# Kernel optimization log

Measured on AMD Instinct MI355X. Metric: run time of the kernel, lower is better.

## Reference

```python
import jax, jax.numpy as jnp
import numpy as np

B, S, H = 1, 2048, 2048
NH = 16
Q_LORA, KV_LORA = 1536, 512
D_NOPE, D_ROPE, D_V = 128, 64, 128
D_QK = D_NOPE + D_ROPE  # 192
EPS = 1e-6
ROPE_BASE = 10000.0


def setup_inputs() -> dict:
    key = jax.random.key(0)
    ks = jax.random.split(key, 8)
    def lin(k, fan_in, fan_out):
        # nn.Linear default init, stored as [in, out] for x @ W
        bound = 1.0 / np.sqrt(fan_in)
        return jax.random.uniform(k, (fan_in, fan_out), jnp.float32, -bound, bound)
    return {
        "hidden_states": jax.random.normal(ks[0], (B, S, H), jnp.float32),
        "Wqa": lin(ks[1], H, Q_LORA),
        "q_a_ln_w": jnp.ones((Q_LORA,), jnp.float32),
        "Wqb": lin(ks[2], Q_LORA, NH * D_QK),
        "Wkva": lin(ks[3], H, KV_LORA + D_ROPE),
        "kv_a_ln_w": jnp.ones((KV_LORA,), jnp.float32),
        "Wkvb": lin(ks[4], KV_LORA, NH * (D_NOPE + D_V)),
        "Wo": lin(ks[5], NH * D_V, H),
    }


def _rmsnorm(x, w):
    xf = x.astype(jnp.float32)
    var = jnp.mean(xf * xf, axis=-1, keepdims=True)
    return w * (xf * jax.lax.rsqrt(var + EPS)).astype(x.dtype)


def _rotate_half(x):
    x1, x2 = jnp.split(x, 2, axis=-1)
    return jnp.concatenate((-x2, x1), axis=-1)


def _rope_tables(seq_len, dtype=jnp.float32):
    inv_freq = 1.0 / (ROPE_BASE ** (jnp.arange(0, D_ROPE, 2, dtype=jnp.float32) / D_ROPE))
    t = jnp.arange(seq_len, dtype=jnp.float32)
    freqs = jnp.outer(t, inv_freq)                      # [S, D_ROPE/2]
    emb = jnp.concatenate((freqs, freqs), axis=-1)      # [S, D_ROPE]
    return jnp.cos(emb).astype(dtype), jnp.sin(emb).astype(dtype)


def reference(hidden_states, Wqa, q_a_ln_w, Wqb, Wkva, kv_a_ln_w, Wkvb, Wo):
    bsz, q_len, _ = hidden_states.shape
    scale = D_QK ** -0.5

    # Q path: LoRA down -> RMSNorm -> up
    q = _rmsnorm(hidden_states @ Wqa, q_a_ln_w) @ Wqb            # [B,S,NH*D_QK]
    q = q.reshape(bsz, q_len, NH, D_QK).transpose(0, 2, 1, 3)    # [B,NH,S,D_QK]
    q_nope, q_pe = q[..., :D_NOPE], q[..., D_NOPE:]

    # KV path: compressed latent + shared rope key
    ckv = hidden_states @ Wkva                                    # [B,S,KV_LORA+D_ROPE]
    compressed_kv, k_pe = ckv[..., :KV_LORA], ckv[..., KV_LORA:]
    k_pe = k_pe.reshape(bsz, q_len, 1, D_ROPE).transpose(0, 2, 1, 3)  # [B,1,S,D_ROPE]
    kv = _rmsnorm(compressed_kv, kv_a_ln_w) @ Wkvb                # [B,S,NH*(D_NOPE+D_V)]
    kv = kv.reshape(bsz, q_len, NH, D_NOPE + D_V).transpose(0, 2, 1, 3)
    k_nope, v = kv[..., :D_NOPE], kv[..., D_NOPE:]                # [B,NH,S,D_NOPE], [B,NH,S,D_V]

    # decoupled RoPE on the rope sub-dims
    cos, sin = _rope_tables(q_len, hidden_states.dtype)
    cos = cos[None, None]  # [1,1,S,D_ROPE] broadcast over batch & heads
    sin = sin[None, None]
    q_pe = q_pe * cos + _rotate_half(q_pe) * sin
    k_pe = k_pe * cos + _rotate_half(k_pe) * sin                  # [B,1,S,D_ROPE]

    query = jnp.concatenate([q_nope, q_pe], axis=-1)              # [B,NH,S,D_QK]
    key = jnp.concatenate([k_nope, jnp.broadcast_to(k_pe, (bsz, NH, q_len, D_ROPE))], axis=-1)

    attn = jnp.einsum('bhqd,bhkd->bhqk', query, key) * scale      # [B,NH,S,S]
    causal = jnp.triu(jnp.ones((q_len, q_len), bool), k=1)
    attn = jnp.where(causal, -jnp.inf, attn)
    attn = jax.nn.softmax(attn.astype(jnp.float32), axis=-1).astype(query.dtype)

    out = jnp.einsum('bhqk,bhkd->bhqd', attn, v)                  # [B,NH,S,D_V]
    out = out.transpose(0, 2, 1, 3).reshape(bsz, q_len, NH * D_V)
    return out @ Wo                                               # [B,S,H]
```

## Files before the change

kernel.cpp:

```cpp
#include <hip/hip_runtime.h>
#include <hip/hip_bf16.h>
#include <math.h>

#define S_LEN 2048
#define H_DIM 2048
#define NH 16
#define Q_LORA 1536
#define KV_LORA 512
#define D_NOPE 128
#define D_ROPE 64
#define D_V 128
#define D_QK 192

typedef unsigned short ushort_t;
typedef __attribute__((ext_vector_type(8))) short short8;
typedef __attribute__((ext_vector_type(4))) float f32x4;

__device__ __forceinline__ ushort_t f2bf(float f) {
    unsigned int u = __float_as_uint(f);
    u = (u + 0x7FFFu + ((u >> 16) & 1u)) >> 16;
    return (ushort_t)u;
}
__device__ __forceinline__ float bf2f(ushort_t u) {
    return __uint_as_float(((unsigned int)u) << 16);
}

__device__ __forceinline__ float exp2_fast(float x) {
    float r;
    asm volatile("v_exp_f32 %0, %1" : "=v"(r) : "v"(x));
    return r;
}

__device__ __forceinline__ void storeC(float* p, float v) { *p = v; }
__device__ __forceinline__ void storeC(ushort_t* p, float v) { *p = f2bf(v); }

__device__ __forceinline__ void gload_lds16(const ushort_t* g, ushort_t* l) {
    __builtin_amdgcn_global_load_lds(
        (const __attribute__((address_space(1))) unsigned int*)(const void*)g,
        (__attribute__((address_space(3))) unsigned int*)(void*)l, 16, 0, 0);
}

__device__ __forceinline__ float dpp_max16(float x) {
    x = fmaxf(x, __int_as_float(__builtin_amdgcn_update_dpp(0, __float_as_int(x), 0xB1, 0xF, 0xF, true)));
    x = fmaxf(x, __int_as_float(__builtin_amdgcn_update_dpp(0, __float_as_int(x), 0x4E, 0xF, 0xF, true)));
    x = fmaxf(x, __int_as_float(__builtin_amdgcn_update_dpp(0, __float_as_int(x), 0x124, 0xF, 0xF, true)));
    x = fmaxf(x, __int_as_float(__builtin_amdgcn_update_dpp(0, __float_as_int(x), 0x128, 0xF, 0xF, true)));
    return x;
}
__device__ __forceinline__ float dpp_sum16(float x) {
    x += __int_as_float(__builtin_amdgcn_update_dpp(0, __float_as_int(x), 0xB1, 0xF, 0xF, true));
    x += __int_as_float(__builtin_amdgcn_update_dpp(0, __float_as_int(x), 0x4E, 0xF, 0xF, true));
    x += __int_as_float(__builtin_amdgcn_update_dpp(0, __float_as_int(x), 0x124, 0xF, 0xF, true));
    x += __int_as_float(__builtin_amdgcn_update_dpp(0, __float_as_int(x), 0x128, 0xF, 0xF, true));
    return x;
}

__device__ __forceinline__ void convT_body(
    const float* __restrict__ W, ushort_t* __restrict__ Wt,
    int K, int N, int n0, int k0, float (*tile)[33])
{
    const int tr = threadIdx.x >> 5, tc = threadIdx.x & 31;
    #pragma unroll
    for (int i = 0; i < 4; ++i) {
        int r = tr + i * 8;
        float v = 0.f;
        if (n0 + tc < N) v = W[(size_t)(k0 + r) * N + n0 + tc];
        tile[r][tc] = v;
    }
    __syncthreads();
    #pragma unroll
    for (int i = 0; i < 4; ++i) {
        int r = tr + i * 8;
        Wt[(size_t)(n0 + r) * K + k0 + tc] = f2bf(tile[tc][r]);
    }
}

__global__ __launch_bounds__(256) void unified_conv(
    const float* __restrict__ hs, ushort_t* __restrict__ hs16,
    const float* __restrict__ Wqa, const float* __restrict__ Wkva,
    const float* __restrict__ Wqb, const float* __restrict__ Wkvb,
    const float* __restrict__ Wo,
    ushort_t* __restrict__ WcatT, ushort_t* __restrict__ WqbT,
    ushort_t* __restrict__ WkvbT, ushort_t* __restrict__ WoT)
{
    __shared__ float tile[32][33];
    int b = blockIdx.x;
    if (b < 4096) {
        int base = (b * 256 + threadIdx.x) * 4;
        float4 v = *(const float4*)(hs + base);
        hs16[base + 0] = f2bf(v.x);
        hs16[base + 1] = f2bf(v.y);
        hs16[base + 2] = f2bf(v.z);
        hs16[base + 3] = f2bf(v.w);
        return;
    }
    b -= 4096;
    const float* W; ushort_t* Wt; int K, N, nbx;
    if (b < 3072)        {            W = Wqa;  Wt = WcatT;                              K = 2048; N = 1536; nbx = 48;  }
    else if (b < 4352)   { b -= 3072; W = Wkva; Wt = WcatT + (size_t)Q_LORA * H_DIM;     K = 2048; N = 576;  nbx = 20;  }
    else if (b < 8960)   { b -= 4352; W = Wqb;  Wt = WqbT;                               K = 1536; N = 3072; nbx = 96;  }
    else if (b < 11008)  { b -= 8960; W = Wkvb; Wt = WkvbT;                              K = 512;  N = 4096; nbx = 128; }
    else                 { b -= 11008; W = Wo;  Wt = WoT;                                K = 2048; N = 2048; nbx = 64;  }
    convT_body(W, Wt, K, N, (b % nbx) * 32, (b / nbx) * 32, tile);
}

__global__ __launch_bounds__(256) void fused_norm_ropek(
    const ushort_t* __restrict__ cat16r, ushort_t* __restrict__ qa16,
    ushort_t* __restrict__ ckv16n, ushort_t* __restrict__ kpe16,
    const float* __restrict__ qlnw, const float* __restrict__ klnw)
{
    __shared__ float red[4];
    const int b = blockIdx.x;
    if (b < 4096) {
        const bool isQ = (b < 2048);
        const int row = isQ ? b : b - 2048;
        const int K = isQ ? Q_LORA : KV_LORA;
        const ushort_t* x = cat16r + (size_t)row * 2176 + (isQ ? 0 : Q_LORA);
        ushort_t* y = (isQ ? qa16 + (size_t)row * Q_LORA : ckv16n + (size_t)row * KV_LORA);
        const float* wv = isQ ? qlnw : klnw;
        float ss = 0.f;
        for (int i = threadIdx.x; i < K; i += 256) { float v = bf2f(x[i]); ss += v * v; }
        #pragma unroll
        for (int off = 32; off > 0; off >>= 1) ss += __shfl_down(ss, off);
        int lane = threadIdx.x & 63, wid = threadIdx.x >> 6;
        if (lane == 0) red[wid] = ss;
        __syncthreads();
        float tot = red[0] + red[1] + red[2] + red[3];
        float rs = rsqrtf(tot / (float)K + 1e-6f);
        for (int i = threadIdx.x; i < K; i += 256)
            y[i] = f2bf(bf2f(x[i]) * rs * wv[i]);
    } else {
        int idx = (b - 4096) * 256 + threadIdx.x;
        if (idx >= S_LEN * 32) return;
        int i = idx & 31;
        int s = idx >> 5;
        float inv = powf(10000.0f, -(2.0f * i) / 64.0f);
        float ang = (float)s * inv;
        float c = cosf(ang), sn = sinf(ang);
        const ushort_t* p = cat16r + (size_t)s * 2176 + Q_LORA + KV_LORA;
        ushort_t* q = kpe16 + (size_t)s * D_ROPE;
        float x1 = bf2f(p[i]), x2 = bf2f(p[i + 32]);
        q[i]      = f2bf(x1 * c - x2 * sn);
        q[i + 32] = f2bf(x2 * c + x1 * sn);
    }
}

__global__ __launch_bounds__(256) void conv_vT_kernel(
    const ushort_t* __restrict__ kv, ushort_t* __restrict__ v16t)
{
    __shared__ ushort_t tile[32][33];
    const int h = blockIdx.z;
    const int s0 = blockIdx.x * 32, d0 = blockIdx.y * 32;
    const int tr = threadIdx.x >> 5, tc = threadIdx.x & 31;
    #pragma unroll
    for (int i = 0; i < 4; ++i) {
        int r = tr + i * 8;
        tile[r][tc] = kv[(size_t)(s0 + r) * 4096 + h * 256 + D_NOPE + d0 + tc];
    }
    __syncthreads();
    #pragma unroll
    for (int i = 0; i < 4; ++i) {
        int r = tr + i * 8;
        v16t[(size_t)h * D_V * S_LEN + (size_t)(d0 + r) * S_LEN + s0 + tc] = tile[tc][r];
    }
}

template <typename CT>
__device__ __forceinline__ void gemm_body_128(
    const ushort_t* __restrict__ A, const ushort_t* __restrict__ Bt,
    CT* __restrict__ C, int N, int K, int m0, int n0,
    ushort_t* Al, ushort_t* Bl)
{
    const int tid = threadIdx.x;
    const int lane = tid & 63;
    const int w = tid >> 6;
    const int lm = lane & 15, quad = lane >> 4;
    const int wr = w >> 1, wc = w & 1;

    f32x4 acc[4][4];
    #pragma unroll
    for (int a = 0; a < 4; ++a)
        #pragma unroll
        for (int b = 0; b < 4; ++b) acc[a][b] = (f32x4){0.f, 0.f, 0.f, 0.f};

    const int rrow = tid >> 2;
    const int rcsw = ((tid & 3) ^ ((tid >> 3) & 3)) * 8;
    const int swq  = quad ^ ((lm >> 1) & 3);

    const int NT = K >> 6;

    auto stage = [&](int buf, int k0) {
        #pragma unroll
        for (int c = 0; c < 2; ++c)
            #pragma unroll
            for (int half = 0; half < 2; ++half) {
                gload_lds16(A + (size_t)(m0 + half * 64 + rrow) * K + k0 + c * 32 + rcsw,
                            Al + buf * 8192 + c * 4096 + half * 2048 + tid * 8);
                gload_lds16(Bt + (size_t)(n0 + half * 64 + rrow) * K + k0 + c * 32 + rcsw,
                            Bl + buf * 8192 + c * 4096 + half * 2048 + tid * 8);
            }
    };

    stage(0, 0);
    stage(1, 64);

    int cur = 0;
    for (int t = 0; t < NT; ++t) {
        if (t + 1 < NT) asm volatile("s_waitcnt vmcnt(8)" ::: "memory");
        else            asm volatile("s_waitcnt vmcnt(0)" ::: "memory");
        __builtin_amdgcn_s_barrier();
        __builtin_amdgcn_sched_barrier(0);

        const ushort_t* Ab = Al + cur * 8192;
        const ushort_t* Bb = Bl + cur * 8192;
        __builtin_amdgcn_s_setprio(1);
        #pragma unroll
        for (int c = 0; c < 2; ++c) {
            short8 af[4], bf[4];
            #pragma unroll
            for (int t2 = 0; t2 < 4; ++t2)
                af[t2] = *(const short8*)(Ab + c * 4096 + (wr * 64 + t2 * 16 + lm) * 32 + swq * 8);
            #pragma unroll
            for (int t2 = 0; t2 < 4; ++t2)
                bf[t2] = *(const short8*)(Bb + c * 4096 + (wc * 64 + t2 * 16 + lm) * 32 + swq * 8);
            #pragma unroll
            for (int mt = 0; mt < 4; ++mt)
                #pragma unroll
                for (int nt = 0; nt < 4; ++nt)
                    acc[mt][nt] = __builtin_amdgcn_mfma_f32_16x16x32_bf16(
                        af[mt], bf[nt], acc[mt][nt], 0, 0, 0);
        }
        __builtin_amdgcn_s_setprio(0);

        __builtin_amdgcn_s_barrier();
        __builtin_amdgcn_sched_barrier(0);
        if (t + 2 < NT) stage(cur, (t + 2) << 6);
        cur ^= 1;
    }

    #pragma unroll
    for (int mt = 0; mt < 4; ++mt)
        #pragma unroll
        for (int nt = 0; nt < 4; ++nt)
            #pragma unroll
            for (int r = 0; r < 4; ++r) {
                int row = m0 + wr * 64 + mt * 16 + quad * 4 + r;
                int col = n0 + wc * 64 + nt * 16 + lm;
                storeC(&C[(size_t)row * N + col], acc[mt][nt][r]);
            }
}

template <typename CT>
__device__ __forceinline__ void gemm_body_128_sb(
    const ushort_t* __restrict__ A, const ushort_t* __restrict__ Bt,
    CT* __restrict__ C, int N, int K, int m0, int n0,
    ushort_t* Al, ushort_t* Bl, float csc)
{
    const int tid = threadIdx.x;
    const int lane = tid & 63;
    const int w = tid >> 6;
    const int lm = lane & 15, quad = lane >> 4;
    const int wr = w >> 1, wc = w & 1;

    f32x4 acc[4][4];
    #pragma unroll
    for (int a = 0; a < 4; ++a)
        #pragma unroll
        for (int b = 0; b < 4; ++b) acc[a][b] = (f32x4){0.f, 0.f, 0.f, 0.f};

    const int rrow = tid >> 2;
    const int rcsw = ((tid & 3) ^ ((tid >> 3) & 3)) * 8;
    const int swq  = quad ^ ((lm >> 1) & 3);

    for (int k0 = 0; k0 < K; k0 += 64) {
        __syncthreads();
        #pragma unroll
        for (int c = 0; c < 2; ++c)
            #pragma unroll
            for (int half = 0; half < 2; ++half) {
                gload_lds16(A + (size_t)(m0 + half * 64 + rrow) * K + k0 + c * 32 + rcsw,
                            Al + c * 4096 + half * 2048 + tid * 8);
                gload_lds16(Bt + (size_t)(n0 + half * 64 + rrow) * K + k0 + c * 32 + rcsw,
                            Bl + c * 4096 + half * 2048 + tid * 8);
            }
        __syncthreads();

        #pragma unroll
        for (int c = 0; c < 2; ++c) {
            short8 af[4], bf[4];
            #pragma unroll
            for (int t2 = 0; t2 < 4; ++t2)
                af[t2] = *(const short8*)(Al + c * 4096 + (wr * 64 + t2 * 16 + lm) * 32 + swq * 8);
            #pragma unroll
            for (int t2 = 0; t2 < 4; ++t2)
                bf[t2] = *(const short8*)(Bl + c * 4096 + (wc * 64 + t2 * 16 + lm) * 32 + swq * 8);
            #pragma unroll
            for (int mt = 0; mt < 4; ++mt)
                #pragma unroll
                for (int nt = 0; nt < 4; ++nt)
                    acc[mt][nt] = __builtin_amdgcn_mfma_f32_16x16x32_bf16(
                        af[mt], bf[nt], acc[mt][nt], 0, 0, 0);
        }
    }

    #pragma unroll
    for (int mt = 0; mt < 4; ++mt)
        #pragma unroll
        for (int nt = 0; nt < 4; ++nt)
            #pragma unroll
            for (int r = 0; r < 4; ++r) {
                int row = m0 + wr * 64 + mt * 16 + quad * 4 + r;
                int col = n0 + wc * 64 + nt * 16 + lm;
                storeC(&C[(size_t)row * N + col], acc[mt][nt][r] * csc);
            }
}

template <typename CT>
__global__ __launch_bounds__(256) void mfma_gemm_bt(
    const ushort_t* __restrict__ A, const ushort_t* __restrict__ Bt,
    CT* __restrict__ C, int N, int K)
{
    __shared__ ushort_t Al[2 * 8192];
    __shared__ ushort_t Bl[2 * 8192];
    gemm_body_128<CT>(A, Bt, C, N, K, blockIdx.y * 128, blockIdx.x * 128, Al, Bl);
}

__global__ __launch_bounds__(256) void mfma_gemm_dual(
    const ushort_t* __restrict__ A1, const ushort_t* __restrict__ Bt1,
    ushort_t* __restrict__ C1, int N1, int K1, int nb1, float sc1,
    const ushort_t* __restrict__ A2, const ushort_t* __restrict__ Bt2,
    ushort_t* __restrict__ C2, int N2, int K2, float sc2)
{
    __shared__ ushort_t Al[8192];
    __shared__ ushort_t Bl[8192];
    int g = blockIdx.x;
    if (g < nb1) {
        int nbx = N1 / 128;
        gemm_body_128_sb<ushort_t>(A1, Bt1, C1, N1, K1, (g / nbx) * 128, (g % nbx) * 128, Al, Bl, sc1);
    } else {
        g -= nb1;
        int nbx = N2 / 128;
        gemm_body_128_sb<ushort_t>(A2, Bt2, C2, N2, K2, (g / nbx) * 128, (g % nbx) * 128, Al, Bl, sc2);
    }
}

template <bool MASKED>
__device__ __forceinline__ void softmax_step_t(
    f32x4 s[4], int k0, int qw, int lm, int quad,
    float m_[4], float l_[4], f32x4 O[8], ushort_t* ps)
{
    float a[4][4];
    float pmax[4];
    float worst = -1e30f;
    #pragma unroll
    for (int r = 0; r < 4; ++r) {
        int qrow = qw + quad * 4 + r;
        #pragma unroll
        for (int st = 0; st < 4; ++st) {
            float v = s[st][r];
            if (MASKED) v = (k0 + st * 16 + lm <= qrow) ? v : -1e30f;
            a[r][st] = v;
        }
        pmax[r] = dpp_max16(fmaxf(fmaxf(fmaxf(a[r][0], a[r][1]), a[r][2]), a[r][3]));
        worst = fmaxf(worst, pmax[r] - m_[r]);
    }
    if (__all(worst <= 11.5f)) {
        #pragma unroll
        for (int r = 0; r < 4; ++r) {
            float p[4];
            #pragma unroll
            for (int st = 0; st < 4; ++st) p[st] = exp2_fast(a[r][st] - m_[r]);
            l_[r] += dpp_sum16((p[0] + p[1]) + (p[2] + p[3]));
            #pragma unroll
            for (int st = 0; st < 4; ++st)
                ps[(quad * 4 + r) * 72 + st * 16 + lm] = f2bf(p[st]);
        }
    } else {
        #pragma unroll
        for (int r = 0; r < 4; ++r) {
            float mn = fmaxf(m_[r], pmax[r]);
            float p[4];
            #pragma unroll
            for (int st = 0; st < 4; ++st) p[st] = exp2_fast(a[r][st] - mn);
            float alpha = exp2_fast(m_[r] - mn);
            float psum = dpp_sum16((p[0] + p[1]) + (p[2] + p[3]));
            l_[r] = l_[r] * alpha + psum;
            m_[r] = mn;
            #pragma unroll
            for (int c = 0; c < 8; ++c) O[c][r] *= alpha;
            #pragma unroll
            for (int st = 0; st < 4; ++st)
                ps[(quad * 4 + r) * 72 + st * 16 + lm] = f2bf(p[st]);
        }
    }
}

__global__ __launch_bounds__(256) void mla_attn_kernel(
    const ushort_t* __restrict__ qb, const ushort_t* __restrict__ kvb,
    const ushort_t* __restrict__ kpe, const ushort_t* __restrict__ v16t,
    ushort_t* __restrict__ aout16)
{
    __shared__ ushort_t Kn[2 * 4 * 64 * 32];
    __shared__ ushort_t Kr[2 * 2 * 64 * 32];
    __shared__ ushort_t Vt[2 * 128 * 32];
    __shared__ ushort_t Ps[4][16 * 72];

    const int o = blockIdx.x;
    const int h = o & 15;
    const int oy = o >> 4;
    const int ty = (oy < 16) ? oy : 47 - oy;
    const int q0 = 64 * (31 - ty);
    const int w = threadIdx.x >> 6;
    const int lane = threadIdx.x & 63;
    const int lm = lane & 15, quad = lane >> 4;
    const int qw = q0 + 16 * w;
    ushort_t* myPs = Ps[w];

    const int skey = lane >> 2;
    const int ssw  = ((lane & 3) ^ ((lane >> 3) & 3)) * 8;
    const int swq  = quad ^ ((lm >> 1) & 3);

    short8 qf[6];
    #pragma unroll
    for (int f = 0; f < 6; ++f)
        qf[f] = *(const short8*)(qb + (size_t)(qw + lm) * 3072 + h * 192 + f * 32 + quad * 8);
    {
        float srow = (float)(qw + lm);
        #pragma unroll
        for (int j = 0; j < 8; ++j) {
            int i = quad * 8 + j;
            float inv = powf(10000.0f, -(2.0f * i) / 64.0f);
            float ang = srow * inv;
            float c = cosf(ang), sn = sinf(ang);
            float x1 = bf2f((ushort_t)qf[4][j]);
            float x2 = bf2f((ushort_t)qf[5][j]);
            qf[4][j] = (short)f2bf(x1 * c - x2 * sn);
            qf[5][j] = (short)f2bf(x2 * c + x1 * sn);
        }
    }
    asm volatile("s_waitcnt vmcnt(0)" ::: "memory");

    f32x4 O[8];
    #pragma unroll
    for (int c = 0; c < 8; ++c) O[c] = (f32x4){0.f, 0.f, 0.f, 0.f};
    float m_[4] = {-1e30f, -1e30f, -1e30f, -1e30f};
    float l_[4] = {0.f, 0.f, 0.f, 0.f};

    auto stageK = [&](int buf, int k0s) {
        #pragma unroll
        for (int i = 0; i < 4; ++i)
            gload_lds16(kvb + (size_t)(k0s + i * 16 + skey) * 4096 + h * 256 + w * 32 + ssw,
                        Kn + buf * 8192 + w * 2048 + i * 512 + lane * 8);
        #pragma unroll
        for (int ii = 0; ii < 2; ++ii) {
            int i = 2 * (w & 1) + ii;
            gload_lds16(kpe + (size_t)(k0s + i * 16 + skey) * 64 + (w >> 1) * 32 + ssw,
                        Kr + buf * 4096 + (w >> 1) * 2048 + i * 512 + lane * 8);
        }
    };
    auto stageV = [&](int k0s) {
        #pragma unroll
        for (int jj = 0; jj < 4; ++jj) {
            int j = 4 * (w >> 1) + jj;
            gload_lds16(v16t + ((size_t)h * 128 + j * 16 + skey) * S_LEN + k0s + (w & 1) * 32 + ssw,
                        Vt + (w & 1) * 4096 + j * 512 + lane * 8);
        }
    };

    const int nt = q0 / 64 + 1;
    stageK(0, 0);

    for (int t = 0; t < nt; ++t) {
        const int k0 = t * 64;
        const bool hasNext = (t + 1 < nt);
        const int kb = t & 1;

        stageV(k0);
        if (hasNext) stageK(kb ^ 1, k0 + 64);

        if (hasNext) asm volatile("s_waitcnt vmcnt(10)" ::: "memory");
        else         asm volatile("s_waitcnt vmcnt(4)"  ::: "memory");
        __builtin_amdgcn_s_barrier();
        __builtin_amdgcn_sched_barrier(0);

        f32x4 s[4];
        #pragma unroll
        for (int st = 0; st < 4; ++st) s[st] = (f32x4){0.f, 0.f, 0.f, 0.f};
        #pragma unroll
        for (int f = 0; f < 4; ++f)
            #pragma unroll
            for (int st = 0; st < 4; ++st) {
                short8 kf = *(const short8*)(Kn + kb * 8192 + f * 2048 + (st * 16 + lm) * 32 + swq * 8);
                s[st] = __builtin_amdgcn_mfma_f32_16x16x32_bf16(qf[f], kf, s[st], 0, 0, 0);
            }
        #pragma unroll
        for (int f2 = 0; f2 < 2; ++f2)
            #pragma unroll
            for (int st = 0; st < 4; ++st) {
                short8 kf = *(const short8*)(Kr + kb * 4096 + f2 * 2048 + (st * 16 + lm) * 32 + swq * 8);
                s[st] = __builtin_amdgcn_mfma_f32_16x16x32_bf16(qf[4 + f2], kf, s[st], 0, 0, 0);
            }

        if (k0 + 63 <= qw) softmax_step_t<false>(s, k0, qw, lm, quad, m_, l_, O, myPs);
        else               softmax_step_t<true >(s, k0, qw, lm, quad, m_, l_, O, myPs);

        if (hasNext) asm volatile("s_waitcnt vmcnt(6) lgkmcnt(0)" ::: "memory");
        else         asm volatile("s_waitcnt vmcnt(0) lgkmcnt(0)" ::: "memory");
        __builtin_amdgcn_s_barrier();
        __builtin_amdgcn_sched_barrier(0);

        short8 pf0 = *(const short8*)(myPs + lm * 72 + quad * 8);
        short8 pf1 = *(const short8*)(myPs + lm * 72 + 32 + quad * 8);
        #pragma unroll
        for (int c = 0; c < 8; ++c) {
            short8 vf0 = *(const short8*)(Vt + (c * 16 + lm) * 32 + swq * 8);
            short8 vf1 = *(const short8*)(Vt + 4096 + (c * 16 + lm) * 32 + swq * 8);
            O[c] = __builtin_amdgcn_mfma_f32_16x16x32_bf16(pf0, vf0, O[c], 0, 0, 0);
            O[c] = __builtin_amdgcn_mfma_f32_16x16x32_bf16(pf1, vf1, O[c], 0, 0, 0);
        }

        __builtin_amdgcn_s_barrier();
        __builtin_amdgcn_sched_barrier(0);
    }

    float linv[4];
    #pragma unroll
    for (int r = 0; r < 4; ++r) linv[r] = __builtin_amdgcn_rcpf(l_[r]);
    #pragma unroll
    for (int c = 0; c < 8; ++c)
        #pragma unroll
        for (int r = 0; r < 4; ++r) {
            int qrow = qw + quad * 4 + r;
            aout16[(size_t)qrow * 2048 + h * D_V + c * 16 + lm] = f2bf(O[c][r] * linv[r]);
        }
}

extern "C" void kernel_launch(void* const* d_in, const int* in_sizes, int n_in,
                              void* d_out, int out_size, void* d_ws, size_t ws_size,
                              hipStream_t stream)
{
    (void)in_sizes; (void)n_in; (void)out_size; (void)ws_size;
    const float* hs   = (const float*)d_in[0];
    const float* Wqa  = (const float*)d_in[1];
    const float* qlnw = (const float*)d_in[2];
    const float* Wqb  = (const float*)d_in[3];
    const float* Wkva = (const float*)d_in[4];
    const float* klnw = (const float*)d_in[5];
    const float* Wkvb = (const float*)d_in[6];
    const float* Wo   = (const float*)d_in[7];
    float* out = (float*)d_out;

    ushort_t* p = (ushort_t*)d_ws;
    ushort_t* hs16   = p; p += (size_t)S_LEN * H_DIM;
    ushort_t* WcatT  = p; p += (size_t)2176 * H_DIM;
    ushort_t* WqbT   = p; p += (size_t)3072 * Q_LORA;
    ushort_t* WkvbT  = p; p += (size_t)4096 * KV_LORA;
    ushort_t* WoT    = p; p += (size_t)H_DIM * H_DIM;
    ushort_t* cat16r = p; p += (size_t)S_LEN * 2176;
    ushort_t* qa16   = p; p += (size_t)S_LEN * Q_LORA;
    ushort_t* qbuf16 = p; p += (size_t)S_LEN * 3072;
    ushort_t* ckv16n = p; p += (size_t)S_LEN * KV_LORA;
    ushort_t* kpe16  = p; p += (size_t)S_LEN * D_ROPE;
    ushort_t* kv16   = p; p += (size_t)S_LEN * 4096;
    ushort_t* v16t   = p; p += (size_t)NH * D_V * S_LEN;
    ushort_t* aout16 = p; p += (size_t)S_LEN * 2048;

    const float QSCALE = 0.0721687836f * 1.44269504f;

    unified_conv<<<19200, 256, 0, stream>>>(
        hs, hs16, Wqa, Wkva, Wqb, Wkvb, Wo, WcatT, WqbT, WkvbT, WoT);
    mfma_gemm_bt<ushort_t><<<dim3(2176 / 128, S_LEN / 128), 256, 0, stream>>>(
        hs16, WcatT, cat16r, 2176, H_DIM);
    fused_norm_ropek<<<4096 + 256, 256, 0, stream>>>(cat16r, qa16, ckv16n, kpe16, qlnw, klnw);
    mfma_gemm_dual<<<384 + 512, 256, 0, stream>>>(
        qa16, WqbT, qbuf16, 3072, Q_LORA, 384, QSCALE,
        ckv16n, WkvbT, kv16, 4096, KV_LORA, 1.0f);
    conv_vT_kernel<<<dim3(S_LEN / 32, D_V / 32, NH), 256, 0, stream>>>(kv16, v16t);
    mla_attn_kernel<<<512, 256, 0, stream>>>(qbuf16, kv16, kpe16, v16t, aout16);
    mfma_gemm_bt<float><<<dim3(H_DIM / 128, S_LEN / 128), 256, 0, stream>>>(
        aout16, WoT, out, H_DIM, H_DIM);
}
```

Baseline: 326.5 us.

## Add XCD-aware GEMM tile mapping and process 32 query rows per attention wave

The GEMM kernels now use a 1D grid and remap block ids so that blocks scheduled on the same XCD work on neighbouring tiles (groups of four M-tiles), aiming for better L2 reuse of A and B panels. The GEMM s_setprio hints are removed. The attention kernel now handles 128 query rows per block, 32 per wave as two 16-row sub-tiles, so each K/V fragment read from LDS is reused across two MFMA chains, and waves past the causal limit skip their compute. The launch drops to 256 blocks, which halves parallelism and loses the previous causal load-balancing pairing of blocks, raising the risk of workload imbalance and higher register pressure.

```diff
diff --git a/kernel.cpp b/kernel.cpp
--- a/kernel.cpp
+++ b/kernel.cpp
@@ -53,6 +53,17 @@
     x += __int_as_float(__builtin_amdgcn_update_dpp(0, __float_as_int(x), 0x124, 0xF, 0xF, true));
     x += __int_as_float(__builtin_amdgcn_update_dpp(0, __float_as_int(x), 0x128, 0xF, 0xF, true));
     return x;
+}
+
+__device__ __forceinline__ void xcd_tile_map(int g, int nwg, int NT, int& mt, int& nt)
+{
+    int q = nwg >> 3, r = nwg & 7;
+    int xcd = g & 7, j = g >> 3;
+    int ng = (xcd < r ? xcd * (q + 1) : r * (q + 1) + (xcd - r) * q) + j;
+    int sr  = ng / (4 * NT);
+    int rem = ng - sr * 4 * NT;
+    nt = rem >> 2;
+    mt = sr * 4 + (rem & 3);
 }
 
 __device__ __forceinline__ void convT_body(
@@ -213,7 +224,6 @@
 
         const ushort_t* Ab = Al + cur * 8192;
         const ushort_t* Bb = Bl + cur * 8192;
-        __builtin_amdgcn_s_setprio(1);
         #pragma unroll
         for (int c = 0; c < 2; ++c) {
             short8 af[4], bf[4];
@@ -230,7 +240,6 @@
                     acc[mt][nt] = __builtin_amdgcn_mfma_f32_16x16x32_bf16(
                         af[mt], bf[nt], acc[mt][nt], 0, 0, 0);
         }
-        __builtin_amdgcn_s_setprio(0);
 
         __builtin_amdgcn_s_barrier();
         __builtin_amdgcn_sched_barrier(0);
@@ -318,11 +327,13 @@
 template <typename CT>
 __global__ __launch_bounds__(256) void mfma_gemm_bt(
     const ushort_t* __restrict__ A, const ushort_t* __restrict__ Bt,
-    CT* __restrict__ C, int N, int K)
+    CT* __restrict__ C, int N, int K, int NTt)
 {
     __shared__ ushort_t Al[2 * 8192];
     __shared__ ushort_t Bl[2 * 8192];
-    gemm_body_128<CT>(A, Bt, C, N, K, blockIdx.y * 128, blockIdx.x * 128, Al, Bl);
+    int mt, nt;
+    xcd_tile_map(blockIdx.x, gridDim.x, NTt, mt, nt);
+    gemm_body_128<CT>(A, Bt, C, N, K, mt * 128, nt * 128, Al, Bl);
 }
 
 __global__ __launch_bounds__(256) void mfma_gemm_dual(
@@ -334,13 +345,14 @@
     __shared__ ushort_t Al[8192];
     __shared__ ushort_t Bl[8192];
     int g = blockIdx.x;
+    int mt, nt;
     if (g < nb1) {
-        int nbx = N1 / 128;
-        gemm_body_128_sb<ushort_t>(A1, Bt1, C1, N1, K1, (g / nbx) * 128, (g % nbx) * 128, Al, Bl, sc1);
+        xcd_tile_map(g, nb1, N1 / 128, mt, nt);
+        gemm_body_128_sb<ushort_t>(A1, Bt1, C1, N1, K1, mt * 128, nt * 128, Al, Bl, sc1);
     } else {
         g -= nb1;
-        int nbx = N2 / 128;
-        gemm_body_128_sb<ushort_t>(A2, Bt2, C2, N2, K2, (g / nbx) * 128, (g % nbx) * 128, Al, Bl, sc2);
+        xcd_tile_map(g, gridDim.x - nb1, N2 / 128, mt, nt);
+        gemm_body_128_sb<ushort_t>(A2, Bt2, C2, N2, K2, mt * 128, nt * 128, Al, Bl, sc2);
     }
 }
 
@@ -400,51 +412,54 @@
     const ushort_t* __restrict__ kpe, const ushort_t* __restrict__ v16t,
     ushort_t* __restrict__ aout16)
 {
-    __shared__ ushort_t Kn[2 * 4 * 64 * 32];
-    __shared__ ushort_t Kr[2 * 2 * 64 * 32];
-    __shared__ ushort_t Vt[2 * 128 * 32];
-    __shared__ ushort_t Ps[4][16 * 72];
+    __shared__ ushort_t Kn[2 * 8192];
+    __shared__ ushort_t Kr[2 * 4096];
+    __shared__ ushort_t Vt[2 * 4096];
+    __shared__ ushort_t Ps[8][16 * 72];
 
     const int o = blockIdx.x;
     const int h = o & 15;
     const int oy = o >> 4;
-    const int ty = (oy < 16) ? oy : 47 - oy;
-    const int q0 = 64 * (31 - ty);
+    const int q0 = 128 * (15 - oy);
     const int w = threadIdx.x >> 6;
     const int lane = threadIdx.x & 63;
     const int lm = lane & 15, quad = lane >> 4;
-    const int qw = q0 + 16 * w;
-    ushort_t* myPs = Ps[w];
+    const int qw = q0 + 32 * w;
 
     const int skey = lane >> 2;
     const int ssw  = ((lane & 3) ^ ((lane >> 3) & 3)) * 8;
     const int swq  = quad ^ ((lm >> 1) & 3);
 
-    short8 qf[6];
-    #pragma unroll
-    for (int f = 0; f < 6; ++f)
-        qf[f] = *(const short8*)(qb + (size_t)(qw + lm) * 3072 + h * 192 + f * 32 + quad * 8);
-    {
-        float srow = (float)(qw + lm);
+    short8 qf[2][6];
+    #pragma unroll
+    for (int qt = 0; qt < 2; ++qt)
+        #pragma unroll
+        for (int f = 0; f < 6; ++f)
+            qf[qt][f] = *(const short8*)(qb + (size_t)(qw + 16 * qt + lm) * 3072 + h * 192 + f * 32 + quad * 8);
+    #pragma unroll
+    for (int qt = 0; qt < 2; ++qt) {
+        float srow = (float)(qw + 16 * qt + lm);
         #pragma unroll
         for (int j = 0; j < 8; ++j) {
             int i = quad * 8 + j;
             float inv = powf(10000.0f, -(2.0f * i) / 64.0f);
             float ang = srow * inv;
             float c = cosf(ang), sn = sinf(ang);
-            float x1 = bf2f((ushort_t)qf[4][j]);
-            float x2 = bf2f((ushort_t)qf[5][j]);
-            qf[4][j] = (short)f2bf(x1 * c - x2 * sn);
-            qf[5][j] = (short)f2bf(x2 * c + x1 * sn);
+            float x1 = bf2f((ushort_t)qf[qt][4][j]);
+            float x2 = bf2f((ushort_t)qf[qt][5][j]);
+            qf[qt][4][j] = (short)f2bf(x1 * c - x2 * sn);
+            qf[qt][5][j] = (short)f2bf(x2 * c + x1 * sn);
         }
     }
     asm volatile("s_waitcnt vmcnt(0)" ::: "memory");
 
-    f32x4 O[8];
-    #pragma unroll
-    for (int c = 0; c < 8; ++c) O[c] = (f32x4){0.f, 0.f, 0.f, 0.f};
-    float m_[4] = {-1e30f, -1e30f, -1e30f, -1e30f};
-    float l_[4] = {0.f, 0.f, 0.f, 0.f};
+    f32x4 O[2][8];
+    #pragma unroll
+    for (int qt = 0; qt < 2; ++qt)
+        #pragma unroll
+        for (int c = 0; c < 8; ++c) O[qt][c] = (f32x4){0.f, 0.f, 0.f, 0.f};
+    float m_[2][4] = {{-1e30f, -1e30f, -1e30f, -1e30f}, {-1e30f, -1e30f, -1e30f, -1e30f}};
+    float l_[2][4] = {{0.f, 0.f, 0.f, 0.f}, {0.f, 0.f, 0.f, 0.f}};
 
     auto stageK = [&](int buf, int k0s) {
         #pragma unroll
@@ -467,7 +482,7 @@
         }
     };
 
-    const int nt = q0 / 64 + 1;
+    const int nt = (q0 >> 6) + 2;
     stageK(0, 0);
 
     for (int t = 0; t < nt; ++t) {
@@ -483,56 +498,79 @@
         __builtin_amdgcn_s_barrier();
         __builtin_amdgcn_sched_barrier(0);
 
-        f32x4 s[4];
-        #pragma unroll
-        for (int st = 0; st < 4; ++st) s[st] = (f32x4){0.f, 0.f, 0.f, 0.f};
-        #pragma unroll
-        for (int f = 0; f < 4; ++f)
-            #pragma unroll
-            for (int st = 0; st < 4; ++st) {
-                short8 kf = *(const short8*)(Kn + kb * 8192 + f * 2048 + (st * 16 + lm) * 32 + swq * 8);
-                s[st] = __builtin_amdgcn_mfma_f32_16x16x32_bf16(qf[f], kf, s[st], 0, 0, 0);
-            }
-        #pragma unroll
-        for (int f2 = 0; f2 < 2; ++f2)
-            #pragma unroll
-            for (int st = 0; st < 4; ++st) {
-                short8 kf = *(const short8*)(Kr + kb * 4096 + f2 * 2048 + (st * 16 + lm) * 32 + swq * 8);
-                s[st] = __builtin_amdgcn_mfma_f32_16x16x32_bf16(qf[4 + f2], kf, s[st], 0, 0, 0);
-            }
-
-        if (k0 + 63 <= qw) softmax_step_t<false>(s, k0, qw, lm, quad, m_, l_, O, myPs);
-        else               softmax_step_t<true >(s, k0, qw, lm, quad, m_, l_, O, myPs);
+        const bool active = (k0 < qw + 32);
+        if (active) {
+            f32x4 s[2][4];
+            #pragma unroll
+            for (int qt = 0; qt < 2; ++qt)
+                #pragma unroll
+                for (int st = 0; st < 4; ++st) s[qt][st] = (f32x4){0.f, 0.f, 0.f, 0.f};
+            #pragma unroll
+            for (int f = 0; f < 4; ++f)
+                #pragma unroll
+                for (int st = 0; st < 4; ++st) {
+                    short8 kf = *(const short8*)(Kn + kb * 8192 + f * 2048 + (st * 16 + lm) * 32 + swq * 8);
+                    s[0][st] = __builtin_amdgcn_mfma_f32_16x16x32_bf16(qf[0][f], kf, s[0][st], 0, 0, 0);
+                    s[1][st] = __builtin_amdgcn_mfma_f32_16x16x32_bf16(qf[1][f], kf, s[1][st], 0, 0, 0);
+                }
+            #pragma unroll
+            for (int f2 = 0; f2 < 2; ++f2)
+                #pragma unroll
+                for (int st = 0; st < 4; ++st) {
+                    short8 kr = *(const short8*)(Kr + kb * 4096 + f2 * 2048 + (st * 16 + lm) * 32 + swq * 8);
+                    s[0][st] = __builtin_amdgcn_mfma_f32_16x16x32_bf16(qf[0][4 + f2], kr, s[0][st], 0, 0, 0);
+                    s[1][st] = __builtin_amdgcn_mfma_f32_16x16x32_bf16(qf[1][4 + f2], kr, s[1][st], 0, 0, 0);
+                }
+
+            #pragma unroll
+            for (int qt = 0; qt < 2; ++qt) {
+                const int base = qw + 16 * qt;
+                if (k0 + 63 <= base) softmax_step_t<false>(s[qt], k0, base, lm, quad, m_[qt], l_[qt], O[qt], Ps[2 * w + qt]);
+                else                 softmax_step_t<true >(s[qt], k0, base, lm, quad, m_[qt], l_[qt], O[qt], Ps[2 * w + qt]);
+            }
+        }
 
         if (hasNext) asm volatile("s_waitcnt vmcnt(6) lgkmcnt(0)" ::: "memory");
         else         asm volatile("s_waitcnt vmcnt(0) lgkmcnt(0)" ::: "memory");
         __builtin_amdgcn_s_barrier();
         __builtin_amdgcn_sched_barrier(0);
 
-        short8 pf0 = *(const short8*)(myPs + lm * 72 + quad * 8);
-        short8 pf1 = *(const short8*)(myPs + lm * 72 + 32 + quad * 8);
-        #pragma unroll
-        for (int c = 0; c < 8; ++c) {
-            short8 vf0 = *(const short8*)(Vt + (c * 16 + lm) * 32 + swq * 8);
-            short8 vf1 = *(const short8*)(Vt + 4096 + (c * 16 + lm) * 32 + swq * 8);
-            O[c] = __builtin_amdgcn_mfma_f32_16x16x32_bf16(pf0, vf0, O[c], 0, 0, 0);
-            O[c] = __builtin_amdgcn_mfma_f32_16x16x32_bf16(pf1, vf1, O[c], 0, 0, 0);
+        if (active) {
+            short8 pf[2][2];
+            #pragma unroll
+            for (int qt = 0; qt < 2; ++qt) {
+                pf[qt][0] = *(const short8*)(Ps[2 * w + qt] + lm * 72 + quad * 8);
+                pf[qt][1] = *(const short8*)(Ps[2 * w + qt] + lm * 72 + 32 + quad * 8);
+            }
+            #pragma unroll
+            for (int c = 0; c < 8; ++c) {
+                short8 vf0 = *(const short8*)(Vt + (c * 16 + lm) * 32 + swq * 8);
+                short8 vf1 = *(const short8*)(Vt + 4096 + (c * 16 + lm) * 32 + swq * 8);
+                #pragma unroll
+                for (int qt = 0; qt < 2; ++qt) {
+                    O[qt][c] = __builtin_amdgcn_mfma_f32_16x16x32_bf16(pf[qt][0], vf0, O[qt][c], 0, 0, 0);
+                    O[qt][c] = __builtin_amdgcn_mfma_f32_16x16x32_bf16(pf[qt][1], vf1, O[qt][c], 0, 0, 0);
+                }
+            }
         }
 
         __builtin_amdgcn_s_barrier();
         __builtin_amdgcn_sched_barrier(0);
     }
 
-    float linv[4];
-    #pragma unroll
-    for (int r = 0; r < 4; ++r) linv[r] = __builtin_amdgcn_rcpf(l_[r]);
-    #pragma unroll
-    for (int c = 0; c < 8; ++c)
-        #pragma unroll
-        for (int r = 0; r < 4; ++r) {
-            int qrow = qw + quad * 4 + r;
-            aout16[(size_t)qrow * 2048 + h * D_V + c * 16 + lm] = f2bf(O[c][r] * linv[r]);
-        }
+    #pragma unroll
+    for (int qt = 0; qt < 2; ++qt) {
+        float linv[4];
+        #pragma unroll
+        for (int r = 0; r < 4; ++r) linv[r] = __builtin_amdgcn_rcpf(l_[qt][r]);
+        #pragma unroll
+        for (int c = 0; c < 8; ++c)
+            #pragma unroll
+            for (int r = 0; r < 4; ++r) {
+                int qrow = qw + 16 * qt + quad * 4 + r;
+                aout16[(size_t)qrow * 2048 + h * D_V + c * 16 + lm] = f2bf(O[qt][c][r] * linv[r]);
+            }
+    }
 }
 
 extern "C" void kernel_launch(void* const* d_in, const int* in_sizes, int n_in,
@@ -569,14 +607,14 @@
 
     unified_conv<<<19200, 256, 0, stream>>>(
         hs, hs16, Wqa, Wkva, Wqb, Wkvb, Wo, WcatT, WqbT, WkvbT, WoT);
-    mfma_gemm_bt<ushort_t><<<dim3(2176 / 128, S_LEN / 128), 256, 0, stream>>>(
-        hs16, WcatT, cat16r, 2176, H_DIM);
+    mfma_gemm_bt<ushort_t><<<16 * 17, 256, 0, stream>>>(
+        hs16, WcatT, cat16r, 2176, H_DIM, 17);
     fused_norm_ropek<<<4096 + 256, 256, 0, stream>>>(cat16r, qa16, ckv16n, kpe16, qlnw, klnw);
     mfma_gemm_dual<<<384 + 512, 256, 0, stream>>>(
         qa16, WqbT, qbuf16, 3072, Q_LORA, 384, QSCALE,
         ckv16n, WkvbT, kv16, 4096, KV_LORA, 1.0f);
     conv_vT_kernel<<<dim3(S_LEN / 32, D_V / 32, NH), 256, 0, stream>>>(kv16, v16t);
-    mla_attn_kernel<<<512, 256, 0, stream>>>(qbuf16, kv16, kpe16, v16t, aout16);
-    mfma_gemm_bt<float><<<dim3(H_DIM / 128, S_LEN / 128), 256, 0, stream>>>(
-        aout16, WoT, out, H_DIM, H_DIM);
-}
+    mla_attn_kernel<<<256, 256, 0, stream>>>(qbuf16, kv16, kpe16, v16t, aout16);
+    mfma_gemm_bt<float><<<16 * 16, 256, 0, stream>>>(
+        aout16, WoT, out, H_DIM, H_DIM, 16);
+}
```

Measured after the change: 369.6 us. 1.13x slower.
